# Kernel tuning notes

Measured on AMD Instinct MI355X. Metric: run time of the kernel, lower is better.

The kernel has to match this reference:

```python
import jax, jax.numpy as jnp
import numpy as np

EPS = 1e-8  # torch.cosine_similarity eps


def _unit(v):
    # normalize over last dim with per-vector eps clamp (torch cosine_similarity semantics)
    n = jnp.sqrt(jnp.sum(v * v, axis=-1, keepdims=True))
    return v / jnp.maximum(n, EPS)


def setup_inputs() -> dict:
    key = jax.random.key(0)
    ks = jax.random.split(key, 10)
    V, D, B, R, S, N, C = 100000, 300, 4096, 32, 32, 2, 2
    return {
        "tokens": jax.random.randint(ks[0], (B, R), 0, V),
        "support_idx": jax.random.randint(ks[1], (N, S), 0, V),
        "emb": jax.random.normal(ks[2], (V, D), jnp.float32) * 0.1,
        "conv1_w": jax.random.normal(ks[3], (2, 2, 3, 3), jnp.float32) * 0.1,
        "conv1_b": jnp.zeros((2,), jnp.float32),
        "conv2_w": jax.random.normal(ks[4], (2, 2, 2, 2), jnp.float32) * 0.1,
        "conv2_b": jnp.zeros((2,), jnp.float32),
        "fc2_w": jax.random.normal(ks[5], (2, 2), jnp.float32) * 0.5,
        "fc2_b": jnp.zeros((2,), jnp.float32),
        "fc_w": jax.random.normal(ks[6], (C, 128), jnp.float32) * 0.1,
        "fc_b": jnp.zeros((C,), jnp.float32),
    }


def reference(tokens, support_idx, emb, conv1_w, conv1_b, conv2_w, conv2_b,
              fc2_w, fc2_b, fc_w, fc_b):
    B = tokens.shape[0]
    # embedding lookups
    x = emb[tokens]          # [B, R, D]
    sv = emb[support_idx]    # [N, S, D]
    # fused normalize + batched matmul = cosine similarity matrix [B, N, S, R]
    sm = jnp.einsum('nsd,brd->bnsr', _unit(sv), _unit(x))
    # original detaches both operands of cosine_similarity
    sm = jax.lax.stop_gradient(sm)
    # channel bi-attention
    flat = sm.reshape(B, 2, -1)                       # [B, 2, S*R]
    attn = jax.nn.softmax(flat, axis=2)
    pooled = jnp.sum(attn * flat, axis=2)             # [B, 2]
    gate = jax.nn.sigmoid(pooled @ fc2_w.T + fc2_b)   # [B, 2]
    h = sm * gate[:, :, None, None]                   # [B, 2, S, R]
    # conv1 3x3 pad 1 + relu + maxpool 2x2
    dn = ('NCHW', 'OIHW', 'NCHW')
    h = jax.lax.conv_general_dilated(h, conv1_w, (1, 1), [(1, 1), (1, 1)],
                                     dimension_numbers=dn)
    h = jax.nn.relu(h + conv1_b[None, :, None, None])
    h = jax.lax.reduce_window(h, -jnp.inf, jax.lax.max,
                              (1, 1, 2, 2), (1, 1, 2, 2), 'VALID')
    # conv2 2x2 pad 1 + relu + avgpool 2x2
    h = jax.lax.conv_general_dilated(h, conv2_w, (1, 1), [(1, 1), (1, 1)],
                                     dimension_numbers=dn)
    h = jax.nn.relu(h + conv2_b[None, :, None, None])
    h = jax.lax.reduce_window(h, 0.0, jax.lax.add,
                              (1, 1, 2, 2), (1, 1, 2, 2), 'VALID') * 0.25
    # dropout is identity at inference; flatten -> [B, 128] -> fc
    h = h.reshape(B, -1)
    return h @ fc_w.T + fc_b
```

## Files before the change

kernel.cpp:

```cpp
#include <hip/hip_runtime.h>
#include <stdint.h>

#define DIM     300
#define NBATCH  4096
#define NSUP    64
#define KP      320
#define ASTF    332
#define SMST    82
#define SMY     36

typedef float f32x4 __attribute__((ext_vector_type(4)));
typedef short s16x8 __attribute__((ext_vector_type(8)));

static __device__ __forceinline__ unsigned bc(float x) { return __builtin_bit_cast(unsigned, x); }
static __device__ __forceinline__ float asf(unsigned u) { return __builtin_bit_cast(float, u); }
static __device__ __forceinline__ unsigned perm_hi(unsigned a, unsigned b) {
    return __builtin_amdgcn_perm(a, b, 0x07060302u);
}
static __device__ __forceinline__ unsigned short f2bf(float x) {
    unsigned u = bc(x);
    return (unsigned short)((u + 0x7FFFu + ((u >> 16) & 1u)) >> 16);
}
static __device__ __forceinline__ float bf2f(unsigned short h) { return asf((unsigned)h << 16); }

struct AB { s16x8 h, l; };
static __device__ __forceinline__ AB cvt_split(float4 c0, float4 c1, float& nrm) {
    nrm = fmaf(c0.x, c0.x, nrm); nrm = fmaf(c0.y, c0.y, nrm);
    nrm = fmaf(c0.z, c0.z, nrm); nrm = fmaf(c0.w, c0.w, nrm);
    nrm = fmaf(c1.x, c1.x, nrm); nrm = fmaf(c1.y, c1.y, nrm);
    nrm = fmaf(c1.z, c1.z, nrm); nrm = fmaf(c1.w, c1.w, nrm);
    const unsigned u0 = bc(c0.x) + 0x8000u, u1 = bc(c0.y) + 0x8000u;
    const unsigned u2 = bc(c0.z) + 0x8000u, u3 = bc(c0.w) + 0x8000u;
    const unsigned u4 = bc(c1.x) + 0x8000u, u5 = bc(c1.y) + 0x8000u;
    const unsigned u6 = bc(c1.z) + 0x8000u, u7 = bc(c1.w) + 0x8000u;
    const float r0 = c0.x - asf(u0 & 0xffff0000u), r1 = c0.y - asf(u1 & 0xffff0000u);
    const float r2 = c0.z - asf(u2 & 0xffff0000u), r3 = c0.w - asf(u3 & 0xffff0000u);
    const float r4 = c1.x - asf(u4 & 0xffff0000u), r5 = c1.y - asf(u5 & 0xffff0000u);
    const float r6 = c1.z - asf(u6 & 0xffff0000u), r7 = c1.w - asf(u7 & 0xffff0000u);
    union { s16x8 v; unsigned u[4]; } H, L;
    H.u[0] = perm_hi(u1, u0); H.u[1] = perm_hi(u3, u2);
    H.u[2] = perm_hi(u5, u4); H.u[3] = perm_hi(u7, u6);
    L.u[0] = perm_hi(bc(r1) + 0x8000u, bc(r0) + 0x8000u);
    L.u[1] = perm_hi(bc(r3) + 0x8000u, bc(r2) + 0x8000u);
    L.u[2] = perm_hi(bc(r5) + 0x8000u, bc(r4) + 0x8000u);
    L.u[3] = perm_hi(bc(r7) + 0x8000u, bc(r6) + 0x8000u);
    AB r; r.h = H.v; r.l = L.v; return r;
}

__global__ __launch_bounds__(64) void prep_kernel(
    const int* __restrict__ sidx, const float* __restrict__ emb,
    unsigned short* __restrict__ Bh, unsigned short* __restrict__ Bl) {
    const int j = blockIdx.x, l = threadIdx.x;
    const size_t tok = (size_t)sidx[j];
    const float* src = emb + tok * DIM;
    float e[5];
    #pragma unroll
    for (int c = 0; c < 5; ++c) {
        const int k = c * 64 + l;
        e[c] = (k < DIM) ? src[k] : 0.f;
    }
    float s = e[0]*e[0] + e[1]*e[1] + e[2]*e[2] + e[3]*e[3] + e[4]*e[4];
    #pragma unroll
    for (int m = 32; m >= 1; m >>= 1) s += __shfl_xor(s, m);
    const float rn = 1.f / fmaxf(sqrtf(s), 1e-8f);
    #pragma unroll
    for (int c = 0; c < 5; ++c) {
        const int k = c * 64 + l;
        const float v = (k < DIM) ? e[c] * rn : 0.f;
        const unsigned short h = f2bf(v);
        Bh[j * KP + k] = h;
        Bl[j * KP + k] = f2bf(v - bf2f(h));
    }
}

__global__ __launch_bounds__(512) void gemm_kernel(
    const int* __restrict__ tokens, const float* __restrict__ emb,
    const unsigned short* __restrict__ Bh, const unsigned short* __restrict__ Bl,
    float* __restrict__ smG) {

    __shared__ __attribute__((aligned(16))) float A[32 * ASTF];

    const int tid = threadIdx.x;
    const int l = tid & 63;
    const int w = tid >> 6;
    const int c = l & 15, hq = l >> 4;
    const int rb = (w >> 2) * 16;
    const int cg = w & 3;
    const int chn = cg >> 1, sb = (cg & 1) * 16;
    const int bbase = blockIdx.x * 8;

    const int ci1 = tid + 512, ci2 = tid + 1024, ci3 = tid + 1536, ci4 = tid + 2048;
    const int r0 = tid / 75, j0 = tid - 75 * r0;
    const int r1 = ci1 / 75, j1 = ci1 - 75 * r1;
    const int r2 = ci2 / 75, j2 = ci2 - 75 * r2;
    const int r3 = ci3 / 75, j3 = ci3 - 75 * r3;
    const int r4 = ci4 / 75, j4 = ci4 - 75 * r4;
    const bool has4 = (ci4 < 2400);

    const unsigned short* pBh = Bh + (cg * 16 + c) * KP + hq * 8;
    const unsigned short* pBl = Bl + (cg * 16 + c) * KP + hq * 8;

    float4 st0, st1, st2, st3, st4;

    {
        const int tb = bbase * 32;
        st0 = *(const float4*)(emb + (size_t)tokens[tb + r0] * DIM + j0 * 4);
        st1 = *(const float4*)(emb + (size_t)tokens[tb + r1] * DIM + j1 * 4);
        st2 = *(const float4*)(emb + (size_t)tokens[tb + r2] * DIM + j2 * 4);
        st3 = *(const float4*)(emb + (size_t)tokens[tb + r3] * DIM + j3 * 4);
        if (has4) st4 = *(const float4*)(emb + (size_t)tokens[tb + r4] * DIM + j4 * 4);
    }
    *(float4*)&A[r0 * ASTF + j0 * 4] = st0;
    *(float4*)&A[r1 * ASTF + j1 * 4] = st1;
    *(float4*)&A[r2 * ASTF + j2 * 4] = st2;
    *(float4*)&A[r3 * ASTF + j3 * 4] = st3;
    if (has4) *(float4*)&A[r4 * ASTF + j4 * 4] = st4;
    __syncthreads();

    #pragma unroll 1
    for (int p = 0; p < 8; ++p) {
        if (p < 7) {
            const int tb = (bbase + p + 1) * 32;
            st0 = *(const float4*)(emb + (size_t)tokens[tb + r0] * DIM + j0 * 4);
            st1 = *(const float4*)(emb + (size_t)tokens[tb + r1] * DIM + j1 * 4);
            st2 = *(const float4*)(emb + (size_t)tokens[tb + r2] * DIM + j2 * 4);
            st3 = *(const float4*)(emb + (size_t)tokens[tb + r3] * DIM + j3 * 4);
            if (has4) st4 = *(const float4*)(emb + (size_t)tokens[tb + r4] * DIM + j4 * 4);
        }

        f32x4 q0 = {0,0,0,0}, q1 = {0,0,0,0}, q2 = {0,0,0,0};
        float nrm = 0.f;
        const float* pA = A + (rb + c) * ASTF + hq * 8;
        #pragma unroll
        for (int t = 0; t < 9; ++t) {
            const float4 c0 = *(const float4*)(pA + t * 32);
            const float4 c1 = *(const float4*)(pA + t * 32 + 4);
            const s16x8 bh = *(const s16x8*)(pBh + t * 32);
            const s16x8 bl = *(const s16x8*)(pBl + t * 32);
            const AB a = cvt_split(c0, c1, nrm);
            q0 = __builtin_amdgcn_mfma_f32_16x16x32_bf16(a.h, bh, q0, 0, 0, 0);
            q1 = __builtin_amdgcn_mfma_f32_16x16x32_bf16(a.h, bl, q1, 0, 0, 0);
            q2 = __builtin_amdgcn_mfma_f32_16x16x32_bf16(a.l, bh, q2, 0, 0, 0);
        }
        {
            const float4 c0 = *(const float4*)(pA + 288);
            const float4 c1 = *(const float4*)(pA + 292);
            float4 d0, d1;
            d0.x = (hq <= 1) ? c0.x : 0.f;
            d0.y = (hq <= 1) ? c0.y : 0.f;
            d0.z = (hq <= 1) ? c0.z : 0.f;
            d0.w = (hq <= 1) ? c0.w : 0.f;
            d1.x = (hq == 0) ? c1.x : 0.f;
            d1.y = (hq == 0) ? c1.y : 0.f;
            d1.z = (hq == 0) ? c1.z : 0.f;
            d1.w = (hq == 0) ? c1.w : 0.f;
            const s16x8 bh = *(const s16x8*)(pBh + 288);
            const s16x8 bl = *(const s16x8*)(pBl + 288);
            const AB a = cvt_split(d0, d1, nrm);
            q0 = __builtin_amdgcn_mfma_f32_16x16x32_bf16(a.h, bh, q0, 0, 0, 0);
            q1 = __builtin_amdgcn_mfma_f32_16x16x32_bf16(a.h, bl, q1, 0, 0, 0);
            q2 = __builtin_amdgcn_mfma_f32_16x16x32_bf16(a.l, bh, q2, 0, 0, 0);
        }

        nrm += __shfl_xor(nrm, 16);
        nrm += __shfl_xor(nrm, 32);
        float4 vv;
        #pragma unroll
        for (int q = 0; q < 4; ++q) {
            const float nq = __shfl(nrm, hq * 4 + q);
            const float rn = __builtin_amdgcn_rcpf(
                fmaxf(__builtin_amdgcn_sqrtf(nq), 1e-8f));
            ((float*)&vv)[q] = (q0[q] + q1[q] + q2[q]) * rn;
        }
        *(float4*)(smG + ((size_t)((bbase + p) * 2 + chn) * 32 + sb + c) * 32 + rb + hq * 4) = vv;

        if (p < 7) {
            __syncthreads();
            *(float4*)&A[r0 * ASTF + j0 * 4] = st0;
            *(float4*)&A[r1 * ASTF + j1 * 4] = st1;
            *(float4*)&A[r2 * ASTF + j2 * 4] = st2;
            *(float4*)&A[r3 * ASTF + j3 * 4] = st3;
            if (has4) *(float4*)&A[r4 * ASTF + j4 * 4] = st4;
            __syncthreads();
        }
    }
}

__global__ __launch_bounds__(256) void tail_kernel(
    const float* __restrict__ smG,
    const float* __restrict__ c1w, const float* __restrict__ c1b,
    const float* __restrict__ c2w, const float* __restrict__ c2b,
    const float* __restrict__ f2w, const float* __restrict__ f2b,
    const float* __restrict__ fcw, const float* __restrict__ fcb,
    float* __restrict__ out) {

    __shared__ __attribute__((aligned(16))) float smP[34 * SMST];
    __shared__ __attribute__((aligned(16))) float pl1P[2 * 17 * 18];
    __shared__ float scrP[8];

    const int tid = threadIdx.x;
    const int w = tid >> 6, l = tid & 63;
    const int b = blockIdx.x;

    {
        const f32x4 z = {0.f, 0.f, 0.f, 0.f};
        #pragma unroll
        for (int i = 0; i < 3; ++i) {
            const int idx = i * 256 + tid;
            if (idx < 697) ((f32x4*)smP)[idx] = z;
        }
        if (tid >= 190) {
            const int z2 = tid - 190;
            const int ic = (z2 >= 33) ? 1 : 0;
            const int rm = z2 - 33 * ic;
            pl1P[ic * 306 + (rm < 17 ? rm : (rm - 16) * 18)] = 0.f;
        }
    }
    __syncthreads();

    {
        const float* src = smG + (size_t)b * 2048;
        float se = 0.f, sv = 0.f;
        #pragma unroll
        for (int h2 = 0; h2 < 2; ++h2) {
            const int f4 = tid * 2 + h2;
            const float4 v = ((const float4*)src)[f4];
            const int base = f4 * 4;
            const int chn = base >> 10;
            const int s = (base >> 5) & 31;
            const int r = base & 31;
            float* dstp = &smP[(r + 1) * SMST + chn * SMY + (s + 1)];
            dstp[0] = v.x; dstp[SMST] = v.y; dstp[2 * SMST] = v.z; dstp[3 * SMST] = v.w;
            const float e0 = __expf(v.x), e1 = __expf(v.y);
            const float e2 = __expf(v.z), e3 = __expf(v.w);
            se += e0 + e1 + e2 + e3;
            sv = fmaf(e0, v.x, sv); sv = fmaf(e1, v.y, sv);
            sv = fmaf(e2, v.z, sv); sv = fmaf(e3, v.w, sv);
        }
        #pragma unroll
        for (int m = 32; m >= 1; m >>= 1) { se += __shfl_xor(se, m); sv += __shfl_xor(sv, m); }
        if (l == 0) { scrP[w] = se; scrP[4 + w] = sv; }
    }
    __syncthreads();

    {
        const int ii = tid >> 4, jj = tid & 15;
        float pc0[4] = {0,0,0,0}, pc1[4] = {0,0,0,0};
        float pA0[4] = {0,0,0,0}, pA1[4] = {0,0,0,0};
        #pragma unroll
        for (int ic = 0; ic < 2; ++ic) {
            float p[4][4];
            #pragma unroll
            for (int a = 0; a < 4; ++a) {
                const int off = (2 * jj + a) * SMST + ic * SMY + 2 * ii;
                const float2 v01 = *(const float2*)&smP[off];
                const float2 v23 = *(const float2*)&smP[off + 2];
                p[a][0] = v01.x; p[a][1] = v01.y; p[a][2] = v23.x; p[a][3] = v23.y;
            }
            #pragma unroll
            for (int py = 0; py < 2; ++py)
            #pragma unroll
            for (int px = 0; px < 2; ++px)
            #pragma unroll
            for (int dy = 0; dy < 3; ++dy)
            #pragma unroll
            for (int dx = 0; dx < 3; ++dx) {
                const float pv = p[px + dx][py + dy];
                const int pos = py * 2 + px;
                if (ic == 0) {
                    pc0[pos] = fmaf(c1w[0 * 9 + dy * 3 + dx], pv, pc0[pos]);
                    pc1[pos] = fmaf(c1w[2 * 9 + dy * 3 + dx], pv, pc1[pos]);
                } else {
                    pA0[pos] = fmaf(c1w[1 * 9 + dy * 3 + dx], pv, pA0[pos]);
                    pA1[pos] = fmaf(c1w[3 * 9 + dy * 3 + dx], pv, pA1[pos]);
                }
            }
        }
        const float p0 = (scrP[4] + scrP[5]) / (scrP[0] + scrP[1]);
        const float p1 = (scrP[6] + scrP[7]) / (scrP[2] + scrP[3]);
        const float gg0 = 1.f / (1.f + __expf(-(f2w[0] * p0 + f2w[1] * p1 + f2b[0])));
        const float gg1 = 1.f / (1.f + __expf(-(f2w[2] * p0 + f2w[3] * p1 + f2b[1])));
        const float b0 = c1b[0], b1 = c1b[1];
        float mx0 = 0.f, mx1 = 0.f;
        #pragma unroll
        for (int i = 0; i < 4; ++i) {
            mx0 = fmaxf(mx0, b0 + gg0 * pc0[i] + gg1 * pA0[i]);
            mx1 = fmaxf(mx1, b1 + gg0 * pc1[i] + gg1 * pA1[i]);
        }
        pl1P[0 * 306 + (ii + 1) * 18 + (jj + 1)] = mx0;
        pl1P[1 * 306 + (ii + 1) * 18 + (jj + 1)] = mx1;
    }
    __syncthreads();

    if (w == 0) {
        float o0 = 0.f, o1 = 0.f;
        #pragma unroll
        for (int h = 0; h < 2; ++h) {
            const int o = h * 64 + l, oc2 = o >> 6, ii2 = (o >> 3) & 7, jj2 = o & 7;
            float sum = 0.f;
            #pragma unroll
            for (int py = 0; py < 2; ++py)
            #pragma unroll
            for (int px = 0; px < 2; ++px) {
                const int y = 2 * ii2 + py, x = 2 * jj2 + px;
                float acc = c2b[oc2];
                #pragma unroll
                for (int ic = 0; ic < 2; ++ic)
                #pragma unroll
                for (int dy = 0; dy < 2; ++dy)
                #pragma unroll
                for (int dx = 0; dx < 2; ++dx)
                    acc += c2w[((oc2 * 2 + ic) * 2 + dy) * 2 + dx] *
                           pl1P[ic * 306 + (y + dy) * 18 + (x + dx)];
                sum += fmaxf(acc, 0.f);
            }
            const float val = 0.25f * sum;
            o0 = fmaf(val, fcw[o], o0);
            o1 = fmaf(val, fcw[128 + o], o1);
        }
        #pragma unroll
        for (int m = 32; m >= 1; m >>= 1) { o0 += __shfl_xor(o0, m); o1 += __shfl_xor(o1, m); }
        if (l == 0) {
            out[b * 2 + 0] = fcb[0] + o0;
            out[b * 2 + 1] = fcb[1] + o1;
        }
    }
}

extern "C" void kernel_launch(void* const* d_in, const int* in_sizes, int n_in,
                              void* d_out, int out_size, void* d_ws, size_t ws_size,
                              hipStream_t stream) {
    const int* tokens = (const int*)d_in[0];
    const int* sidx   = (const int*)d_in[1];
    const float* emb  = (const float*)d_in[2];
    const float* c1w  = (const float*)d_in[3];
    const float* c1b  = (const float*)d_in[4];
    const float* c2w  = (const float*)d_in[5];
    const float* c2b  = (const float*)d_in[6];
    const float* f2w  = (const float*)d_in[7];
    const float* f2b  = (const float*)d_in[8];
    const float* fcw  = (const float*)d_in[9];
    const float* fcb  = (const float*)d_in[10];

    float* smG = (float*)d_ws;
    unsigned short* Bh = (unsigned short*)((char*)d_ws + (size_t)NBATCH * 2048 * 4);
    unsigned short* Bl = Bh + NSUP * KP;

    prep_kernel<<<NSUP, 64, 0, stream>>>(sidx, emb, Bh, Bl);
    gemm_kernel<<<512, 512, 0, stream>>>(tokens, emb, Bh, Bl, smG);
    tail_kernel<<<NBATCH, 256, 0, stream>>>(smG, c1w, c1b, c2w, c2b,
                                            f2w, f2b, fcw, fcb, (float*)d_out);
}
```

Before: 83.10 us.

## Pre-split A to bf16 hi/lo in LDS, compute row norms via MFMA

The fp32-to-bf16 hi/lo split of the gathered embedding rows now happens once when they are written to shared memory, instead of in every wave's MFMA loop. This removes repeated conversion work, since four waves previously re-split the same rows. Row squared norms now come from two extra MFMAs (ah·ah and ah·al) on the diagonal, replacing scalar FMAs and shuffles, and are passed through an LDS array. The grid doubles to 1024 blocks of 4 batches each, and s_setprio is added around the MFMA loop. The costs are extra MFMA work, a slightly less exact norm (the lo·lo term is dropped), and a norm exchange through LDS that relies on only an lgkmcnt wait rather than a barrier.

```diff
diff --git a/kernel.cpp b/kernel.cpp
--- a/kernel.cpp
+++ b/kernel.cpp
@@ -5,9 +5,11 @@
 #define NBATCH  4096
 #define NSUP    64
 #define KP      320
-#define ASTF    332
+#define ASTRIDE 328
 #define SMST    82
 #define SMY     36
+#define GRID_G  1024
+#define PPB     4
 
 typedef float f32x4 __attribute__((ext_vector_type(4)));
 typedef short s16x8 __attribute__((ext_vector_type(8)));
@@ -22,30 +24,6 @@
     return (unsigned short)((u + 0x7FFFu + ((u >> 16) & 1u)) >> 16);
 }
 static __device__ __forceinline__ float bf2f(unsigned short h) { return asf((unsigned)h << 16); }
-
-struct AB { s16x8 h, l; };
-static __device__ __forceinline__ AB cvt_split(float4 c0, float4 c1, float& nrm) {
-    nrm = fmaf(c0.x, c0.x, nrm); nrm = fmaf(c0.y, c0.y, nrm);
-    nrm = fmaf(c0.z, c0.z, nrm); nrm = fmaf(c0.w, c0.w, nrm);
-    nrm = fmaf(c1.x, c1.x, nrm); nrm = fmaf(c1.y, c1.y, nrm);
-    nrm = fmaf(c1.z, c1.z, nrm); nrm = fmaf(c1.w, c1.w, nrm);
-    const unsigned u0 = bc(c0.x) + 0x8000u, u1 = bc(c0.y) + 0x8000u;
-    const unsigned u2 = bc(c0.z) + 0x8000u, u3 = bc(c0.w) + 0x8000u;
-    const unsigned u4 = bc(c1.x) + 0x8000u, u5 = bc(c1.y) + 0x8000u;
-    const unsigned u6 = bc(c1.z) + 0x8000u, u7 = bc(c1.w) + 0x8000u;
-    const float r0 = c0.x - asf(u0 & 0xffff0000u), r1 = c0.y - asf(u1 & 0xffff0000u);
-    const float r2 = c0.z - asf(u2 & 0xffff0000u), r3 = c0.w - asf(u3 & 0xffff0000u);
-    const float r4 = c1.x - asf(u4 & 0xffff0000u), r5 = c1.y - asf(u5 & 0xffff0000u);
-    const float r6 = c1.z - asf(u6 & 0xffff0000u), r7 = c1.w - asf(u7 & 0xffff0000u);
-    union { s16x8 v; unsigned u[4]; } H, L;
-    H.u[0] = perm_hi(u1, u0); H.u[1] = perm_hi(u3, u2);
-    H.u[2] = perm_hi(u5, u4); H.u[3] = perm_hi(u7, u6);
-    L.u[0] = perm_hi(bc(r1) + 0x8000u, bc(r0) + 0x8000u);
-    L.u[1] = perm_hi(bc(r3) + 0x8000u, bc(r2) + 0x8000u);
-    L.u[2] = perm_hi(bc(r5) + 0x8000u, bc(r4) + 0x8000u);
-    L.u[3] = perm_hi(bc(r7) + 0x8000u, bc(r6) + 0x8000u);
-    AB r; r.h = H.v; r.l = L.v; return r;
-}
 
 __global__ __launch_bounds__(64) void prep_kernel(
     const int* __restrict__ sidx, const float* __restrict__ emb,
@@ -78,7 +56,9 @@
     const unsigned short* __restrict__ Bh, const unsigned short* __restrict__ Bl,
     float* __restrict__ smG) {
 
-    __shared__ __attribute__((aligned(16))) float A[32 * ASTF];
+    __shared__ __attribute__((aligned(16))) unsigned short Ah[32 * ASTRIDE];
+    __shared__ __attribute__((aligned(16))) unsigned short Al[32 * ASTRIDE];
+    __shared__ __attribute__((aligned(16))) float norms[32];
 
     const int tid = threadIdx.x;
     const int l = tid & 63;
@@ -87,7 +67,13 @@
     const int rb = (w >> 2) * 16;
     const int cg = w & 3;
     const int chn = cg >> 1, sb = (cg & 1) * 16;
-    const int bbase = blockIdx.x * 8;
+    const int bbase = blockIdx.x * PPB;
+
+    if (tid < 448) {
+        const int row = tid / 14, q = tid - 14 * row;
+        ((unsigned*)Ah)[row * 164 + 150 + q] = 0u;
+        ((unsigned*)Al)[row * 164 + 150 + q] = 0u;
+    }
 
     const int ci1 = tid + 512, ci2 = tid + 1024, ci3 = tid + 1536, ci4 = tid + 2048;
     const int r0 = tid / 75, j0 = tid - 75 * r0;
@@ -99,6 +85,7 @@
 
     const unsigned short* pBh = Bh + (cg * 16 + c) * KP + hq * 8;
     const unsigned short* pBl = Bl + (cg * 16 + c) * KP + hq * 8;
+    const int abase = (rb + c) * ASTRIDE + hq * 8;
 
     float4 st0, st1, st2, st3, st4;
 
@@ -110,16 +97,30 @@
         st3 = *(const float4*)(emb + (size_t)tokens[tb + r3] * DIM + j3 * 4);
         if (has4) st4 = *(const float4*)(emb + (size_t)tokens[tb + r4] * DIM + j4 * 4);
     }
-    *(float4*)&A[r0 * ASTF + j0 * 4] = st0;
-    *(float4*)&A[r1 * ASTF + j1 * 4] = st1;
-    *(float4*)&A[r2 * ASTF + j2 * 4] = st2;
-    *(float4*)&A[r3 * ASTF + j3 * 4] = st3;
-    if (has4) *(float4*)&A[r4 * ASTF + j4 * 4] = st4;
+
+    #define STORE_CHUNK(ST, R, J)                                                   \
+    {                                                                               \
+        const unsigned u0 = bc(ST.x) + 0x8000u, u1 = bc(ST.y) + 0x8000u;            \
+        const unsigned u2 = bc(ST.z) + 0x8000u, u3 = bc(ST.w) + 0x8000u;            \
+        const float q0f = ST.x - asf(u0 & 0xffff0000u);                             \
+        const float q1f = ST.y - asf(u1 & 0xffff0000u);                             \
+        const float q2f = ST.z - asf(u2 & 0xffff0000u);                             \
+        const float q3f = ST.w - asf(u3 & 0xffff0000u);                             \
+        *(uint2*)(&Ah[(R) * ASTRIDE + (J) * 4]) =                                   \
+            uint2{perm_hi(u1, u0), perm_hi(u3, u2)};                                \
+        *(uint2*)(&Al[(R) * ASTRIDE + (J) * 4]) =                                   \
+            uint2{perm_hi(bc(q1f) + 0x8000u, bc(q0f) + 0x8000u),                    \
+                  perm_hi(bc(q3f) + 0x8000u, bc(q2f) + 0x8000u)};                   \
+    }
+
+    STORE_CHUNK(st0, r0, j0); STORE_CHUNK(st1, r1, j1); STORE_CHUNK(st2, r2, j2);
+    STORE_CHUNK(st3, r3, j3);
+    if (has4) STORE_CHUNK(st4, r4, j4);
     __syncthreads();
 
     #pragma unroll 1
-    for (int p = 0; p < 8; ++p) {
-        if (p < 7) {
+    for (int p = 0; p < PPB; ++p) {
+        if (p < PPB - 1) {
             const int tb = (bbase + p + 1) * 32;
             st0 = *(const float4*)(emb + (size_t)tokens[tb + r0] * DIM + j0 * 4);
             st1 = *(const float4*)(emb + (size_t)tokens[tb + r1] * DIM + j1 * 4);
@@ -129,61 +130,48 @@
         }
 
         f32x4 q0 = {0,0,0,0}, q1 = {0,0,0,0}, q2 = {0,0,0,0};
-        float nrm = 0.f;
-        const float* pA = A + (rb + c) * ASTF + hq * 8;
-        #pragma unroll
-        for (int t = 0; t < 9; ++t) {
-            const float4 c0 = *(const float4*)(pA + t * 32);
-            const float4 c1 = *(const float4*)(pA + t * 32 + 4);
+        f32x4 gv = {0,0,0,0}, g2 = {0,0,0,0};
+        __builtin_amdgcn_s_setprio(1);
+        #pragma unroll
+        for (int t = 0; t < 10; ++t) {
+            const s16x8 ah = *(const s16x8*)(Ah + abase + t * 32);
+            const s16x8 al = *(const s16x8*)(Al + abase + t * 32);
             const s16x8 bh = *(const s16x8*)(pBh + t * 32);
             const s16x8 bl = *(const s16x8*)(pBl + t * 32);
-            const AB a = cvt_split(c0, c1, nrm);
-            q0 = __builtin_amdgcn_mfma_f32_16x16x32_bf16(a.h, bh, q0, 0, 0, 0);
-            q1 = __builtin_amdgcn_mfma_f32_16x16x32_bf16(a.h, bl, q1, 0, 0, 0);
-            q2 = __builtin_amdgcn_mfma_f32_16x16x32_bf16(a.l, bh, q2, 0, 0, 0);
-        }
-        {
-            const float4 c0 = *(const float4*)(pA + 288);
-            const float4 c1 = *(const float4*)(pA + 292);
-            float4 d0, d1;
-            d0.x = (hq <= 1) ? c0.x : 0.f;
-            d0.y = (hq <= 1) ? c0.y : 0.f;
-            d0.z = (hq <= 1) ? c0.z : 0.f;
-            d0.w = (hq <= 1) ? c0.w : 0.f;
-            d1.x = (hq == 0) ? c1.x : 0.f;
-            d1.y = (hq == 0) ? c1.y : 0.f;
-            d1.z = (hq == 0) ? c1.z : 0.f;
-            d1.w = (hq == 0) ? c1.w : 0.f;
-            const s16x8 bh = *(const s16x8*)(pBh + 288);
-            const s16x8 bl = *(const s16x8*)(pBl + 288);
-            const AB a = cvt_split(d0, d1, nrm);
-            q0 = __builtin_amdgcn_mfma_f32_16x16x32_bf16(a.h, bh, q0, 0, 0, 0);
-            q1 = __builtin_amdgcn_mfma_f32_16x16x32_bf16(a.h, bl, q1, 0, 0, 0);
-            q2 = __builtin_amdgcn_mfma_f32_16x16x32_bf16(a.l, bh, q2, 0, 0, 0);
-        }
-
-        nrm += __shfl_xor(nrm, 16);
-        nrm += __shfl_xor(nrm, 32);
+            q0 = __builtin_amdgcn_mfma_f32_16x16x32_bf16(ah, bh, q0, 0, 0, 0);
+            q1 = __builtin_amdgcn_mfma_f32_16x16x32_bf16(ah, bl, q1, 0, 0, 0);
+            q2 = __builtin_amdgcn_mfma_f32_16x16x32_bf16(al, bh, q2, 0, 0, 0);
+            gv = __builtin_amdgcn_mfma_f32_16x16x32_bf16(ah, ah, gv, 0, 0, 0);
+            g2 = __builtin_amdgcn_mfma_f32_16x16x32_bf16(ah, al, g2, 0, 0, 0);
+        }
+        __builtin_amdgcn_s_setprio(0);
+
+        if (hq == (c >> 2)) {
+            const int q = c & 3;
+            const float d1 = (q == 0) ? gv[0] : (q == 1) ? gv[1] : (q == 2) ? gv[2] : gv[3];
+            const float d2 = (q == 0) ? g2[0] : (q == 1) ? g2[1] : (q == 2) ? g2[2] : g2[3];
+            norms[rb + c] = d1 + 2.f * d2;
+        }
+        asm volatile("s_waitcnt lgkmcnt(0)" ::: "memory");
+        const f32x4 n4 = *(const f32x4*)&norms[rb + hq * 4];
         float4 vv;
         #pragma unroll
         for (int q = 0; q < 4; ++q) {
-            const float nq = __shfl(nrm, hq * 4 + q);
             const float rn = __builtin_amdgcn_rcpf(
-                fmaxf(__builtin_amdgcn_sqrtf(nq), 1e-8f));
+                fmaxf(__builtin_amdgcn_sqrtf(n4[q]), 1e-8f));
             ((float*)&vv)[q] = (q0[q] + q1[q] + q2[q]) * rn;
         }
         *(float4*)(smG + ((size_t)((bbase + p) * 2 + chn) * 32 + sb + c) * 32 + rb + hq * 4) = vv;
 
-        if (p < 7) {
+        if (p < PPB - 1) {
             __syncthreads();
-            *(float4*)&A[r0 * ASTF + j0 * 4] = st0;
-            *(float4*)&A[r1 * ASTF + j1 * 4] = st1;
-            *(float4*)&A[r2 * ASTF + j2 * 4] = st2;
-            *(float4*)&A[r3 * ASTF + j3 * 4] = st3;
-            if (has4) *(float4*)&A[r4 * ASTF + j4 * 4] = st4;
+            STORE_CHUNK(st0, r0, j0); STORE_CHUNK(st1, r1, j1); STORE_CHUNK(st2, r2, j2);
+            STORE_CHUNK(st3, r3, j3);
+            if (has4) STORE_CHUNK(st4, r4, j4);
             __syncthreads();
         }
     }
+    #undef STORE_CHUNK
 }
 
 __global__ __launch_bounds__(256) void tail_kernel(
@@ -347,7 +335,7 @@
     unsigned short* Bl = Bh + NSUP * KP;
 
     prep_kernel<<<NSUP, 64, 0, stream>>>(sidx, emb, Bh, Bl);
-    gemm_kernel<<<512, 512, 0, stream>>>(tokens, emb, Bh, Bl, smG);
+    gemm_kernel<<<GRID_G, 512, 0, stream>>>(tokens, emb, Bh, Bl, smG);
     tail_kernel<<<NBATCH, 256, 0, stream>>>(smG, c1w, c1b, c2w, c2b,
                                             f2w, f2b, fcw, fcb, (float*)d_out);
 }
```

Result: no change. 84.44 us (+1.6%).

## Stage support matrix in LDS and stream token rows directly from global

Applied to the files above, without the earlier changes.

The GEMM kernel no longer stages the gathered embedding rows in shared memory behind block-wide barriers. It loads the bf16 hi/lo support matrix (64x320) into LDS once per block. Each wave then reads its 16 token rows directly from global memory into registers and computes all four 16-column support groups, so each A fragment is reused across 12 MFMAs. The grid shrinks to 256 blocks, each looping over 4 tiles per wave. This removes the per-iteration __syncthreads and the LDS round trip for A, at the cost of more accumulator registers and uncoalesced global reads for A with no prefetch.

```diff
diff --git a/kernel.cpp b/kernel.cpp
--- a/kernel.cpp
+++ b/kernel.cpp
@@ -5,9 +5,11 @@
 #define NBATCH  4096
 #define NSUP    64
 #define KP      320
-#define ASTF    332
+#define LSTR    328
 #define SMST    82
 #define SMY     36
+#define GRID_G  256
+#define NTILE   8192
 
 typedef float f32x4 __attribute__((ext_vector_type(4)));
 typedef short s16x8 __attribute__((ext_vector_type(8)));
@@ -78,110 +80,94 @@
     const unsigned short* __restrict__ Bh, const unsigned short* __restrict__ Bl,
     float* __restrict__ smG) {
 
-    __shared__ __attribute__((aligned(16))) float A[32 * ASTF];
+    __shared__ __attribute__((aligned(16))) unsigned short BhL[NSUP * LSTR];
+    __shared__ __attribute__((aligned(16))) unsigned short BlL[NSUP * LSTR];
 
     const int tid = threadIdx.x;
     const int l = tid & 63;
     const int w = tid >> 6;
     const int c = l & 15, hq = l >> 4;
-    const int rb = (w >> 2) * 16;
-    const int cg = w & 3;
-    const int chn = cg >> 1, sb = (cg & 1) * 16;
-    const int bbase = blockIdx.x * 8;
-
-    const int ci1 = tid + 512, ci2 = tid + 1024, ci3 = tid + 1536, ci4 = tid + 2048;
-    const int r0 = tid / 75, j0 = tid - 75 * r0;
-    const int r1 = ci1 / 75, j1 = ci1 - 75 * r1;
-    const int r2 = ci2 / 75, j2 = ci2 - 75 * r2;
-    const int r3 = ci3 / 75, j3 = ci3 - 75 * r3;
-    const int r4 = ci4 / 75, j4 = ci4 - 75 * r4;
-    const bool has4 = (ci4 < 2400);
-
-    const unsigned short* pBh = Bh + (cg * 16 + c) * KP + hq * 8;
-    const unsigned short* pBl = Bl + (cg * 16 + c) * KP + hq * 8;
-
-    float4 st0, st1, st2, st3, st4;
-
-    {
-        const int tb = bbase * 32;
-        st0 = *(const float4*)(emb + (size_t)tokens[tb + r0] * DIM + j0 * 4);
-        st1 = *(const float4*)(emb + (size_t)tokens[tb + r1] * DIM + j1 * 4);
-        st2 = *(const float4*)(emb + (size_t)tokens[tb + r2] * DIM + j2 * 4);
-        st3 = *(const float4*)(emb + (size_t)tokens[tb + r3] * DIM + j3 * 4);
-        if (has4) st4 = *(const float4*)(emb + (size_t)tokens[tb + r4] * DIM + j4 * 4);
-    }
-    *(float4*)&A[r0 * ASTF + j0 * 4] = st0;
-    *(float4*)&A[r1 * ASTF + j1 * 4] = st1;
-    *(float4*)&A[r2 * ASTF + j2 * 4] = st2;
-    *(float4*)&A[r3 * ASTF + j3 * 4] = st3;
-    if (has4) *(float4*)&A[r4 * ASTF + j4 * 4] = st4;
+
+    #pragma unroll
+    for (int m = 0; m < 10; ++m) {
+        const int ci = tid + m * 512;
+        const int plane = ci / 2560;
+        const int rem = ci - plane * 2560;
+        const int rr = rem / 40, jc = rem - rr * 40;
+        const uint4 v = *(const uint4*)((plane ? Bl : Bh) + rr * KP + jc * 8);
+        *(uint4*)((plane ? BlL : BhL) + rr * LSTR + jc * 8) = v;
+    }
     __syncthreads();
 
+    const int bbl0 = c * LSTR + hq * 8;
+
     #pragma unroll 1
-    for (int p = 0; p < 8; ++p) {
-        if (p < 7) {
-            const int tb = (bbase + p + 1) * 32;
-            st0 = *(const float4*)(emb + (size_t)tokens[tb + r0] * DIM + j0 * 4);
-            st1 = *(const float4*)(emb + (size_t)tokens[tb + r1] * DIM + j1 * 4);
-            st2 = *(const float4*)(emb + (size_t)tokens[tb + r2] * DIM + j2 * 4);
-            st3 = *(const float4*)(emb + (size_t)tokens[tb + r3] * DIM + j3 * 4);
-            if (has4) st4 = *(const float4*)(emb + (size_t)tokens[tb + r4] * DIM + j4 * 4);
-        }
-
-        f32x4 q0 = {0,0,0,0}, q1 = {0,0,0,0}, q2 = {0,0,0,0};
+    for (int i = 0; i < NTILE / (GRID_G * 8); ++i) {
+        const int tile = blockIdx.x * 8 + w + i * (GRID_G * 8);
+        const size_t tok = (size_t)tokens[tile * 16 + c];
+        const float* srcA = emb + tok * DIM;
+
+        f32x4 q0[4] = {{0,0,0,0},{0,0,0,0},{0,0,0,0},{0,0,0,0}};
+        f32x4 q1[4] = {{0,0,0,0},{0,0,0,0},{0,0,0,0},{0,0,0,0}};
+        f32x4 q2[4] = {{0,0,0,0},{0,0,0,0},{0,0,0,0},{0,0,0,0}};
         float nrm = 0.f;
-        const float* pA = A + (rb + c) * ASTF + hq * 8;
+
         #pragma unroll
         for (int t = 0; t < 9; ++t) {
-            const float4 c0 = *(const float4*)(pA + t * 32);
-            const float4 c1 = *(const float4*)(pA + t * 32 + 4);
-            const s16x8 bh = *(const s16x8*)(pBh + t * 32);
-            const s16x8 bl = *(const s16x8*)(pBl + t * 32);
+            const float4 c0 = *(const float4*)(srcA + t * 32 + hq * 8);
+            const float4 c1 = *(const float4*)(srcA + t * 32 + hq * 8 + 4);
             const AB a = cvt_split(c0, c1, nrm);
-            q0 = __builtin_amdgcn_mfma_f32_16x16x32_bf16(a.h, bh, q0, 0, 0, 0);
-            q1 = __builtin_amdgcn_mfma_f32_16x16x32_bf16(a.h, bl, q1, 0, 0, 0);
-            q2 = __builtin_amdgcn_mfma_f32_16x16x32_bf16(a.l, bh, q2, 0, 0, 0);
+            #pragma unroll
+            for (int cg = 0; cg < 4; ++cg) {
+                const s16x8 bh = *(const s16x8*)(BhL + cg * 16 * LSTR + bbl0 + t * 32);
+                const s16x8 bl = *(const s16x8*)(BlL + cg * 16 * LSTR + bbl0 + t * 32);
+                q0[cg] = __builtin_amdgcn_mfma_f32_16x16x32_bf16(a.h, bh, q0[cg], 0, 0, 0);
+                q1[cg] = __builtin_amdgcn_mfma_f32_16x16x32_bf16(a.h, bl, q1[cg], 0, 0, 0);
+                q2[cg] = __builtin_amdgcn_mfma_f32_16x16x32_bf16(a.l, bh, q2[cg], 0, 0, 0);
+            }
         }
         {
-            const float4 c0 = *(const float4*)(pA + 288);
-            const float4 c1 = *(const float4*)(pA + 292);
+            const float* pc = srcA + ((hq == 0) ? 288 : 292);
+            const float4 c0 = *(const float4*)(pc);
+            const float4 c1 = *(const float4*)(pc + 4);
             float4 d0, d1;
-            d0.x = (hq <= 1) ? c0.x : 0.f;
-            d0.y = (hq <= 1) ? c0.y : 0.f;
-            d0.z = (hq <= 1) ? c0.z : 0.f;
-            d0.w = (hq <= 1) ? c0.w : 0.f;
+            d0.x = (hq == 0) ? c0.x : ((hq == 1) ? c1.x : 0.f);
+            d0.y = (hq == 0) ? c0.y : ((hq == 1) ? c1.y : 0.f);
+            d0.z = (hq == 0) ? c0.z : ((hq == 1) ? c1.z : 0.f);
+            d0.w = (hq == 0) ? c0.w : ((hq == 1) ? c1.w : 0.f);
             d1.x = (hq == 0) ? c1.x : 0.f;
             d1.y = (hq == 0) ? c1.y : 0.f;
             d1.z = (hq == 0) ? c1.z : 0.f;
             d1.w = (hq == 0) ? c1.w : 0.f;
-            const s16x8 bh = *(const s16x8*)(pBh + 288);
-            const s16x8 bl = *(const s16x8*)(pBl + 288);
             const AB a = cvt_split(d0, d1, nrm);
-            q0 = __builtin_amdgcn_mfma_f32_16x16x32_bf16(a.h, bh, q0, 0, 0, 0);
-            q1 = __builtin_amdgcn_mfma_f32_16x16x32_bf16(a.h, bl, q1, 0, 0, 0);
-            q2 = __builtin_amdgcn_mfma_f32_16x16x32_bf16(a.l, bh, q2, 0, 0, 0);
+            #pragma unroll
+            for (int cg = 0; cg < 4; ++cg) {
+                const s16x8 bh = *(const s16x8*)(BhL + cg * 16 * LSTR + bbl0 + 288);
+                const s16x8 bl = *(const s16x8*)(BlL + cg * 16 * LSTR + bbl0 + 288);
+                q0[cg] = __builtin_amdgcn_mfma_f32_16x16x32_bf16(a.h, bh, q0[cg], 0, 0, 0);
+                q1[cg] = __builtin_amdgcn_mfma_f32_16x16x32_bf16(a.h, bl, q1[cg], 0, 0, 0);
+                q2[cg] = __builtin_amdgcn_mfma_f32_16x16x32_bf16(a.l, bh, q2[cg], 0, 0, 0);
+            }
         }
 
         nrm += __shfl_xor(nrm, 16);
         nrm += __shfl_xor(nrm, 32);
-        float4 vv;
+        float rn[4];
         #pragma unroll
         for (int q = 0; q < 4; ++q) {
             const float nq = __shfl(nrm, hq * 4 + q);
-            const float rn = __builtin_amdgcn_rcpf(
+            rn[q] = __builtin_amdgcn_rcpf(
                 fmaxf(__builtin_amdgcn_sqrtf(nq), 1e-8f));
-            ((float*)&vv)[q] = (q0[q] + q1[q] + q2[q]) * rn;
-        }
-        *(float4*)(smG + ((size_t)((bbase + p) * 2 + chn) * 32 + sb + c) * 32 + rb + hq * 4) = vv;
-
-        if (p < 7) {
-            __syncthreads();
-            *(float4*)&A[r0 * ASTF + j0 * 4] = st0;
-            *(float4*)&A[r1 * ASTF + j1 * 4] = st1;
-            *(float4*)&A[r2 * ASTF + j2 * 4] = st2;
-            *(float4*)&A[r3 * ASTF + j3 * 4] = st3;
-            if (has4) *(float4*)&A[r4 * ASTF + j4 * 4] = st4;
-            __syncthreads();
+        }
+        const int b = tile >> 1, hf = tile & 1;
+        #pragma unroll
+        for (int cg = 0; cg < 4; ++cg) {
+            const int ch = cg >> 1, s = (cg & 1) * 16 + c;
+            float4 vv;
+            #pragma unroll
+            for (int q = 0; q < 4; ++q)
+                ((float*)&vv)[q] = (q0[cg][q] + q1[cg][q] + q2[cg][q]) * rn[q];
+            *(float4*)(smG + ((size_t)(b * 2 + ch) * 32 + s) * 32 + hf * 16 + hq * 4) = vv;
         }
     }
 }
@@ -347,7 +333,7 @@
     unsigned short* Bl = Bh + NSUP * KP;
 
     prep_kernel<<<NSUP, 64, 0, stream>>>(sidx, emb, Bh, Bl);
-    gemm_kernel<<<512, 512, 0, stream>>>(tokens, emb, Bh, Bl, smG);
+    gemm_kernel<<<GRID_G, 512, 0, stream>>>(tokens, emb, Bh, Bl, smG);
     tail_kernel<<<NBATCH, 256, 0, stream>>>(smG, c1w, c1b, c2w, c2b,
                                             f2w, f2b, fcw, fcb, (float*)d_out);
 }
```

New measurement: 144.9 us. 74.4% more time.
